# Kernel tuning notes

Measured on AMD Instinct MI355X. Metric: run time of the kernel, lower is better.

Reference implementation:

```python
import jax, jax.numpy as jnp
import numpy as np

R = 5          # output_size of AdaptiveMaxPool1d (init default)
B = 2048       # batch
T = 8192       # padded max sequence length


def setup_inputs() -> dict:
    key = jax.random.key(0)
    k1, k2 = jax.random.split(key)
    inputs = jax.random.normal(k1, (B, T), dtype=jnp.float32)
    # lengths in [R, T] so each of the R adaptive windows is non-empty
    lengths = jax.random.randint(k2, (B,), R, T + 1)
    return {"inputs": inputs, "lengths": lengths}


def _minmax(inputs, lengths, r_out=R):
    """Vectorized ragged AdaptiveMaxPool1d(+min via -pool(-x)) then sort.

    PyTorch AdaptiveMaxPool1d window r over a length-L signal:
      start = floor(r*L/R), end = ceil((r+1)*L/R)
    """
    _, t_max = inputs.shape
    t = jnp.arange(t_max)              # [T]
    L = lengths[:, None]               # [B,1]
    pos_inf = jnp.asarray(jnp.inf, inputs.dtype)
    maxes, mins = [], []
    for r in range(r_out):             # fixed small loop over R windows
        start = (r * L) // r_out                       # [B,1]
        end = ((r + 1) * L + r_out - 1) // r_out       # [B,1], <= L
        mask = (t >= start) & (t < end)                # [B,T]
        maxes.append(jnp.max(jnp.where(mask, inputs, -pos_inf), axis=1))
        mins.append(jnp.min(jnp.where(mask, inputs, pos_inf), axis=1))
    out = jnp.stack(maxes + mins, axis=1)  # [B, 2R]: cat([top, neg]) per sample
    return jnp.sort(out, axis=1)           # ascending, like torch .sort()


def reference(inputs, lengths):
    return _minmax(inputs, lengths)
```

## Files before the change

kernel.cpp:

```cpp
#include <hip/hip_runtime.h>

#define RWIN 5
#define TMAX 8192

__global__ __launch_bounds__(5 * 64) void minmax_sort_kernel(
    const float* __restrict__ in, const int* __restrict__ lengths,
    float* __restrict__ out)
{
    __shared__ float sm[2 * RWIN];

    const int b    = blockIdx.x;
    const int tid  = threadIdx.x;
    const int w    = tid >> 6;
    const int lane = tid & 63;

    const int L = lengths[b];
    const float* rowp = in + (size_t)b * TMAX;

    const int s  = (w * L) / RWIN;
    const int e  = ((w + 1) * L + (RWIN - 1)) / RWIN;
    const int sa = s & ~3;
    const int niter = (e - sa + 255) >> 8;

    const float NINF = -__builtin_inff();
    const float PINF =  __builtin_inff();
    const int t0 = sa + lane * 4;

    float4 v[7];
    #pragma unroll
    for (int i = 0; i < 7; ++i) {
        if (i < niter) {
            const int t = t0 + (i << 8);
            v[i] = *reinterpret_cast<const float4*>(rowp + (t < e ? t : sa));
        }
    }

    float mx = NINF, mn = PINF;
    #pragma unroll
    for (int i = 0; i < 7; ++i) {
        if (i < niter) {
            if (i > 0 && i < niter - 1) {
                mx = fmaxf(mx, fmaxf(fmaxf(v[i].x, v[i].y), fmaxf(v[i].z, v[i].w)));
                mn = fminf(mn, fminf(fminf(v[i].x, v[i].y), fminf(v[i].z, v[i].w)));
            } else {
                const int t = t0 + (i << 8);
                const float xs[4] = {v[i].x, v[i].y, v[i].z, v[i].w};
                #pragma unroll
                for (int j = 0; j < 4; ++j) {
                    const int  idx = t + j;
                    const bool ok  = (idx >= s) & (idx < e);
                    mx = fmaxf(mx, ok ? xs[j] : NINF);
                    mn = fminf(mn, ok ? xs[j] : PINF);
                }
            }
        }
    }

    #pragma unroll
    for (int off = 1; off < 64; off <<= 1) {
        mx = fmaxf(mx, __shfl_xor(mx, off));
        mn = fminf(mn, __shfl_xor(mn, off));
    }
    if (lane == 0) { sm[w] = mx; sm[RWIN + w] = mn; }
    __syncthreads();

    if (tid < 2 * RWIN) {
        const float vv = sm[tid];
        int pos = 0;
        #pragma unroll
        for (int j = 0; j < 2 * RWIN; ++j) {
            const float vj = sm[j];
            pos += (int)((vj < vv) | ((vj == vv) & (j < tid)));
        }
        out[b * (2 * RWIN) + pos] = vv;
    }
}

extern "C" void kernel_launch(void* const* d_in, const int* in_sizes, int n_in,
                              void* d_out, int out_size, void* d_ws, size_t ws_size,
                              hipStream_t stream) {
    const float* in      = (const float*)d_in[0];
    const int*   lengths = (const int*)d_in[1];
    float*       out     = (float*)d_out;
    const int B = in_sizes[1];
    minmax_sort_kernel<<<B, 5 * 64, 0, stream>>>(in, lengths, out);
}
```

Baseline: 11.32 us.

## Split window reduction and rank sort into two kernels with decoupled tasks

Window min/max moves into its own kernel where each wavefront handles one (row, window) task, eight tasks per 512-thread block, and the ordering puts the same window of consecutive rows together. Results go to a workspace buffer, and a second small kernel does the 10-element rank sort per row. This drops the per-block __syncthreads and the idle-thread sort tail, and balances load across blocks. In exchange it adds a second kernel launch and a round trip through global memory.

Result: slower. 14.20 us (+25.4%).

```diff
diff --git a/kernel.cpp b/kernel.cpp
--- a/kernel.cpp
+++ b/kernel.cpp
@@ -2,23 +2,22 @@
 
 #define RWIN 5
 #define TMAX 8192
+#define NROW 2048
 
-__global__ __launch_bounds__(5 * 64) void minmax_sort_kernel(
+__global__ __launch_bounds__(512) void window_minmax_kernel(
     const float* __restrict__ in, const int* __restrict__ lengths,
-    float* __restrict__ out)
+    float* __restrict__ ws)
 {
-    __shared__ float sm[2 * RWIN];
+    const int tid  = threadIdx.x;
+    const int lane = tid & 63;
+    const int task = blockIdx.x * 8 + (tid >> 6);
+    const int row  = task & (NROW - 1);
+    const int win  = task >> 11;
 
-    const int b    = blockIdx.x;
-    const int tid  = threadIdx.x;
-    const int w    = tid >> 6;
-    const int lane = tid & 63;
-
-    const int L = lengths[b];
-    const float* rowp = in + (size_t)b * TMAX;
-
-    const int s  = (w * L) / RWIN;
-    const int e  = ((w + 1) * L + (RWIN - 1)) / RWIN;
+    const int L = lengths[row];
+    const float* rowp = in + (size_t)row * TMAX;
+    const int s  = (win * L) / RWIN;
+    const int e  = ((win + 1) * L + (RWIN - 1)) / RWIN;
     const int sa = s & ~3;
     const int niter = (e - sa + 255) >> 8;
 
@@ -61,19 +60,28 @@
         mx = fmaxf(mx, __shfl_xor(mx, off));
         mn = fminf(mn, __shfl_xor(mn, off));
     }
-    if (lane == 0) { sm[w] = mx; sm[RWIN + w] = mn; }
-    __syncthreads();
+    if (lane == 0) {
+        ws[row * (2 * RWIN) + win]        = mx;
+        ws[row * (2 * RWIN) + RWIN + win] = mn;
+    }
+}
 
-    if (tid < 2 * RWIN) {
-        const float vv = sm[tid];
-        int pos = 0;
-        #pragma unroll
-        for (int j = 0; j < 2 * RWIN; ++j) {
-            const float vj = sm[j];
-            pos += (int)((vj < vv) | ((vj == vv) & (j < tid)));
-        }
-        out[b * (2 * RWIN) + pos] = vv;
+__global__ __launch_bounds__(256) void rank_sort_kernel(
+    const float* __restrict__ ws, float* __restrict__ out, int n)
+{
+    const int g = blockIdx.x * 256 + threadIdx.x;
+    if (g >= n) return;
+    const int row = g / (2 * RWIN);
+    const int j   = g % (2 * RWIN);
+    const float* base = ws + row * (2 * RWIN);
+    const float v = base[j];
+    int pos = 0;
+    #pragma unroll
+    for (int k = 0; k < 2 * RWIN; ++k) {
+        const float vk = base[k];
+        pos += (int)((vk < v) | ((vk == v) & (k < j)));
     }
+    out[row * (2 * RWIN) + pos] = v;
 }
 
 extern "C" void kernel_launch(void* const* d_in, const int* in_sizes, int n_in,
@@ -82,6 +90,11 @@
     const float* in      = (const float*)d_in[0];
     const int*   lengths = (const int*)d_in[1];
     float*       out     = (float*)d_out;
-    const int B = in_sizes[1];
-    minmax_sort_kernel<<<B, 5 * 64, 0, stream>>>(in, lengths, out);
+    float*       ws      = (float*)d_ws;
+
+    const int ntask = NROW * RWIN;
+    window_minmax_kernel<<<ntask / 8, 512, 0, stream>>>(in, lengths, ws);
+
+    const int n = NROW * 2 * RWIN;
+    rank_sort_kernel<<<(n + 255) / 256, 256, 0, stream>>>(ws, out, n);
 }
```
